# Performance work log

Hardware: AMD Instinct MI355X
Metric: run time of the kernel (lower is better)

## Reference

```python
import jax, jax.numpy as jnp
import numpy as np

N, E, G = 50000, 800000, 128
F_IN, H, NHID, C = 310, 128, 64, 2  # H = 2*nhid
NEG_SLOPE = 0.2


def setup_inputs() -> dict:
    key = jax.random.key(0)
    ks = jax.random.split(key, 16)
    def lin(k, fan_in, shape):
        return (jax.random.normal(k, shape, jnp.float32) / np.sqrt(fan_in)).astype(jnp.float32)
    return {
        "x": jax.random.normal(ks[0], (N, F_IN), jnp.float32),
        "edge_index": jax.random.randint(ks[1], (2, E), 0, N, dtype=jnp.int32),
        "batch": jnp.sort(jax.random.randint(ks[2], (N,), 0, G, dtype=jnp.int32)),
        "W1": lin(ks[3], F_IN, (F_IN, H)),
        "a_src1": lin(ks[4], H, (H,)),
        "a_dst1": lin(ks[5], H, (H,)),
        "b1": jnp.zeros((H,), jnp.float32),
        "W2": lin(ks[6], H, (H, H)),
        "a_src2": lin(ks[7], H, (H,)),
        "a_dst2": lin(ks[8], H, (H,)),
        "b2": jnp.zeros((H,), jnp.float32),
        "fc1_w": lin(ks[9], H, (H, NHID)),
        "fc1_b": jnp.zeros((NHID,), jnp.float32),
        "fc2_w": lin(ks[10], NHID, (NHID, C)),
        "fc2_b": jnp.zeros((C,), jnp.float32),
    }


def _gat(x, src, dst, W, a_src, a_dst, b):
    # PyG GATConv, heads=1: h = xW; e_ij = LeakyReLU(a_src.h_j + a_dst.h_i)
    h = x @ W                               # [N, H]
    asrc = h @ a_src                        # [N]
    adst = h @ a_dst                        # [N]
    e = jax.nn.leaky_relu(asrc[src] + adst[dst], NEG_SLOPE)  # [E']
    # segment softmax over incoming edges of each target node
    m = jax.ops.segment_max(e, dst, num_segments=N)
    ex = jnp.exp(e - m[dst])
    s = jax.ops.segment_sum(ex, dst, num_segments=N)
    w = ex / s[dst]                         # [E']
    out = jax.ops.segment_sum(h[src] * w[:, None], dst, num_segments=N)
    return out + b


def reference(x, edge_index, batch, W1, a_src1, a_dst1, b1,
              W2, a_src2, a_dst2, b2, fc1_w, fc1_b, fc2_w, fc2_b):
    # add self loops (GATConv default add_self_loops=True)
    ar = jnp.arange(N, dtype=edge_index.dtype)
    src = jnp.concatenate([edge_index[0], ar])
    dst = jnp.concatenate([edge_index[1], ar])

    h = jax.nn.selu(_gat(x, src, dst, W1, a_src1, a_dst1, b1))
    h = jax.nn.selu(_gat(h, src, dst, W2, a_src2, a_dst2, b2))

    # global mean pool over graphs
    summed = jax.ops.segment_sum(h, batch, num_segments=G)          # [G, H]
    cnt = jax.ops.segment_sum(jnp.ones((N,), h.dtype), batch, num_segments=G)
    pooled = jax.nn.selu(summed / jnp.maximum(cnt, 1.0)[:, None])

    z = jax.nn.selu(pooled @ fc1_w + fc1_b)  # dropout is identity in eval
    logits = z @ fc2_w + fc2_b
    return jax.nn.log_softmax(logits, axis=-1)
```

## Files before the change

kernel.cpp:

```cpp
#include <hip/hip_runtime.h>
#include <hip/hip_bf16.h>
#include <math.h>

#define NN 50000
#define NE 800000
#define NET (NE + NN)
#define FIN 310
#define HD 128
#define NHID 64
#define NCLS 2
#define NG 128
#define NEG_SLOPE 0.2f
#define KP1 320
#define KP2 128

#define SLOTS 64
#define NPART 8
#define PART_SZ (NN / NPART)
#define EPB 4096
#define NSLICE ((NET + EPB - 1) / EPB)
#define NSC (NSLICE * NPART)
#define GB1 ((NN + 63) / 64)

#define SELU_SCALE 1.0507009873554804934193349852946f
#define SELU_ALPHA 1.6732632423543772848170429916717f

typedef short bf16x8 __attribute__((ext_vector_type(8)));
typedef float f32x4 __attribute__((ext_vector_type(4)));

__device__ __forceinline__ float selu(float x) {
    return SELU_SCALE * (x > 0.f ? x : SELU_ALPHA * (__expf(x) - 1.f));
}
__device__ __forceinline__ float lrelu(float x) {
    return x > 0.f ? x : NEG_SLOPE * x;
}
__device__ __forceinline__ unsigned short f2bf(float f) {
    unsigned int u = __float_as_uint(f);
    u = (u + 0x7fffu + ((u >> 16) & 1u)) >> 16;
    return (unsigned short)u;
}
__device__ __forceinline__ float bf2f(unsigned short b) {
    return __uint_as_float(((unsigned int)b) << 16);
}


__global__ void k_castW(const float* __restrict__ W1, const float* __restrict__ W2,
                        unsigned short* __restrict__ W1p, unsigned short* __restrict__ W2p,
                        int* __restrict__ cursor) {
    int i = blockIdx.x * blockDim.x + threadIdx.x;
    if (i < NN) cursor[i] = 0;
    const int N1 = HD * KP1;
    if (i < N1) {
        int n = i / KP1, k = i % KP1;
        unsigned short v = (k < FIN) ? f2bf(W1[(size_t)k * HD + n]) : (unsigned short)0;
        W1p[((k >> 3) * HD + n) * 8 + (k & 7)] = v;
    } else {
        int j = i - N1;
        if (j < HD * KP2) {
            int n = j / KP2, k = j % KP2;
            W2p[((k >> 3) * HD + n) * 8 + (k & 7)] = f2bf(W2[(size_t)k * HD + n]);
        }
    }
}


#define RGEMM_EPILOGUE                                                         \
    int gr_base = r0 + w * 16 + quad * 4;                                      \
    _Pragma("unroll")                                                          \
    for (int r = 0; r < 4; ++r) {                                              \
        int gr = gr_base + r;                                                  \
        if (gr < M) {                                                          \
            _Pragma("unroll")                                                  \
            for (int nt = 0; nt < 8; ++nt)                                     \
                C[(size_t)gr * HD + nt * 16 + l16] = f2bf(acc[nt][r]);         \
        }                                                                      \
    }                                                                          \
    _Pragma("unroll")                                                          \
    for (int r = 0; r < 4; ++r) {                                              \
        float s1 = 0.f, s2 = 0.f;                                              \
        _Pragma("unroll")                                                      \
        for (int nt = 0; nt < 8; ++nt) {                                       \
            int c = nt * 16 + l16;                                             \
            float v = acc[nt][r];                                              \
            s1 += v * a_src[c];                                                \
            s2 += v * a_dst[c];                                                \
        }                                                                      \
        _Pragma("unroll")                                                      \
        for (int off = 1; off < 16; off <<= 1) {                               \
            s1 += __shfl_xor(s1, off);                                         \
            s2 += __shfl_xor(s2, off);                                         \
        }                                                                      \
        int gr = gr_base + r;                                                  \
        if (l16 == 0 && gr < M) { asrcp[gr] = s1; adstp[gr] = s2; }            \
    }


__global__ __launch_bounds__(256) void k_pre(const float* __restrict__ A,
                                             const unsigned short* __restrict__ Bp,
                                             unsigned short* __restrict__ C,
                                             float* __restrict__ asrcp,
                                             float* __restrict__ adstp,
                                             const float* __restrict__ a_src,
                                             const float* __restrict__ a_dst,
                                             int M,
                                             const int* __restrict__ ei,
                                             int* __restrict__ cursor,
                                             unsigned short* __restrict__ slots) {
    if (blockIdx.x >= GB1) {
        int b = blockIdx.x - GB1;
        int part = b & (NPART - 1);
        int slice = b >> 3;
        int lo = part * PART_SZ;
        int base = slice * EPB + threadIdx.x;
#pragma unroll
        for (int k = 0; k < EPB / 256; ++k) {
            int i = base + k * 256;
            if (i >= NET) break;
            int d = (i < NE) ? ei[NE + i] : (i - NE);
            if ((unsigned)(d - lo) < (unsigned)PART_SZ) {
                int s = (i < NE) ? ei[i] : d;
                int pos = atomicAdd(&cursor[d], 1) & (SLOTS - 1);
                slots[(size_t)d * SLOTS + pos] = (unsigned short)s;
            }
        }
        return;
    }
    int t = threadIdx.x;
    int lane = t & 63, w = t >> 6;
    int quad = lane >> 4, l16 = lane & 15;
    int r0 = blockIdx.x * 64;

    int grow = r0 + w * 16 + l16;
    int arow = min(grow, M - 1);
    const float* aptr = A + (size_t)arow * FIN + quad * 8;

    f32x4 acc[8] = {};
#pragma unroll 2
    for (int k0 = 0; k0 < 288; k0 += 32) {
        const float* ap = aptr + k0;
        float2 f0 = *(const float2*)(ap + 0);
        float2 f1 = *(const float2*)(ap + 2);
        float2 f2 = *(const float2*)(ap + 4);
        float2 f3 = *(const float2*)(ap + 6);
        union { bf16x8 v; unsigned short u[8]; } af;
        af.u[0] = f2bf(f0.x); af.u[1] = f2bf(f0.y);
        af.u[2] = f2bf(f1.x); af.u[3] = f2bf(f1.y);
        af.u[4] = f2bf(f2.x); af.u[5] = f2bf(f2.y);
        af.u[6] = f2bf(f3.x); af.u[7] = f2bf(f3.y);
        const unsigned short* bbase = Bp + ((size_t)(k0 >> 3) + quad) * (HD * 8) + l16 * 8;
#pragma unroll
        for (int nt = 0; nt < 8; ++nt) {
            bf16x8 bfr = *(const bf16x8*)(bbase + nt * 128);
            acc[nt] = __builtin_amdgcn_mfma_f32_16x16x32_bf16(af.v, bfr, acc[nt], 0, 0, 0);
        }
    }
    {
        int kb = 288 + quad * 8;
        union { bf16x8 v; unsigned short u[8]; } af;
#pragma unroll
        for (int j = 0; j < 8; ++j)
            af.u[j] = (kb + j < FIN) ? f2bf(aptr[288 + j]) : (unsigned short)0;
        const unsigned short* bbase = Bp + ((size_t)(288 >> 3) + quad) * (HD * 8) + l16 * 8;
#pragma unroll
        for (int nt = 0; nt < 8; ++nt) {
            bf16x8 bfr = *(const bf16x8*)(bbase + nt * 128);
            acc[nt] = __builtin_amdgcn_mfma_f32_16x16x32_bf16(af.v, bfr, acc[nt], 0, 0, 0);
        }
    }
    RGEMM_EPILOGUE
}


__global__ __launch_bounds__(256) void k_gemm2(const unsigned short* __restrict__ A,
                                               const unsigned short* __restrict__ Bp,
                                               unsigned short* __restrict__ C,
                                               float* __restrict__ asrcp,
                                               float* __restrict__ adstp,
                                               const float* __restrict__ a_src,
                                               const float* __restrict__ a_dst,
                                               int M) {
    int t = threadIdx.x;
    int lane = t & 63, w = t >> 6;
    int quad = lane >> 4, l16 = lane & 15;
    int r0 = blockIdx.x * 64;

    int grow = r0 + w * 16 + l16;
    int arow = min(grow, M - 1);
    const unsigned short* aptr = A + (size_t)arow * KP2 + quad * 8;

    f32x4 acc[8] = {};
#pragma unroll
    for (int k0 = 0; k0 < KP2; k0 += 32) {
        bf16x8 af = *(const bf16x8*)(aptr + k0);
        const unsigned short* bbase = Bp + ((size_t)(k0 >> 3) + quad) * (HD * 8) + l16 * 8;
#pragma unroll
        for (int nt = 0; nt < 8; ++nt) {
            bf16x8 bfr = *(const bf16x8*)(bbase + nt * 128);
            acc[nt] = __builtin_amdgcn_mfma_f32_16x16x32_bf16(af, bfr, acc[nt], 0, 0, 0);
        }
    }
    RGEMM_EPILOGUE
}


__global__ __launch_bounds__(256) void k_gat(const unsigned short* __restrict__ h,
                                             const float* __restrict__ asrc,
                                             const float* __restrict__ adst,
                                             const int* __restrict__ degv,
                                             const unsigned short* __restrict__ slots,
                                             const float* __restrict__ bias,
                                             unsigned short* __restrict__ out) {
    int node = blockIdx.x * 4 + (threadIdx.x >> 6);
    int lane = threadIdx.x & 63;
    if (node >= NN) return;
    int g = lane >> 4, cl = lane & 15;
    int deg = degv[node];
    float adsti = adst[node];

    float2 acc2[4] = {};

    int cnt = min(deg, SLOTS);
    int s_c = 0; float p_c = 0.f;
    if (lane < cnt) {
        s_c = slots[(size_t)node * SLOTS + lane];
        p_c = __expf(lrelu(asrc[s_c] + adsti));
    }
    float den_l = p_c;
    int nt = (cnt + 3) >> 2;
    for (int t = 0; t < nt; t += 2) {
        float pv[2]; uint4 hv[2];
#pragma unroll
        for (int u = 0; u < 2; ++u) {
            int tt = t + u;
            bool valid = tt < nt;
            int e = (4 * tt + g) & 63;
            int s = __shfl(s_c, e);
            float p = __shfl(p_c, e);
            int sa = valid ? s : 0;
            pv[u] = valid ? p : 0.f;
            hv[u] = *(const uint4*)(h + (size_t)sa * HD + cl * 8);
        }
#pragma unroll
        for (int u = 0; u < 2; ++u) {
            float p = pv[u];
            unsigned int w0 = hv[u].x, w1 = hv[u].y, w2 = hv[u].z, w3 = hv[u].w;
            acc2[0].x += p * __uint_as_float(w0 << 16);
            acc2[0].y += p * __uint_as_float(w0 & 0xffff0000u);
            acc2[1].x += p * __uint_as_float(w1 << 16);
            acc2[1].y += p * __uint_as_float(w1 & 0xffff0000u);
            acc2[2].x += p * __uint_as_float(w2 << 16);
            acc2[2].y += p * __uint_as_float(w2 & 0xffff0000u);
            acc2[3].x += p * __uint_as_float(w3 << 16);
            acc2[3].y += p * __uint_as_float(w3 & 0xffff0000u);
        }
    }
#pragma unroll
    for (int k = 0; k < 4; ++k) {
        acc2[k].x += __shfl_xor(acc2[k].x, 16);
        acc2[k].y += __shfl_xor(acc2[k].y, 16);
        acc2[k].x += __shfl_xor(acc2[k].x, 32);
        acc2[k].y += __shfl_xor(acc2[k].y, 32);
    }
#pragma unroll
    for (int off = 32; off; off >>= 1)
        den_l += __shfl_xor(den_l, off);

    if (g == 0) {
        float inv = 1.f / den_l;
        int c0 = cl * 8;
        float4 b0 = *(const float4*)(bias + c0);
        float4 b1 = *(const float4*)(bias + c0 + 4);
        float v0 = selu(acc2[0].x * inv + b0.x);
        float v1 = selu(acc2[0].y * inv + b0.y);
        float v2 = selu(acc2[1].x * inv + b0.z);
        float v3 = selu(acc2[1].y * inv + b0.w);
        float v4 = selu(acc2[2].x * inv + b1.x);
        float v5 = selu(acc2[2].y * inv + b1.y);
        float v6 = selu(acc2[3].x * inv + b1.z);
        float v7 = selu(acc2[3].y * inv + b1.w);
        uint4 pk;
        pk.x = (unsigned int)f2bf(v0) | ((unsigned int)f2bf(v1) << 16);
        pk.y = (unsigned int)f2bf(v2) | ((unsigned int)f2bf(v3) << 16);
        pk.z = (unsigned int)f2bf(v4) | ((unsigned int)f2bf(v5) << 16);
        pk.w = (unsigned int)f2bf(v6) | ((unsigned int)f2bf(v7) << 16);
        *(uint4*)(out + (size_t)node * HD + c0) = pk;
    }
}


__device__ __forceinline__ int lower_bound_i(const int* a, int n, int key) {
    int lo = 0, hi = n;
    while (lo < hi) {
        int mid = (lo + hi) >> 1;
        if (a[mid] < key) lo = mid + 1; else hi = mid;
    }
    return lo;
}

__global__ __launch_bounds__(512) void k_poolfc(const unsigned short* __restrict__ x,
                                                const int* __restrict__ batch,
                                                const float* __restrict__ w1,
                                                const float* __restrict__ b1,
                                                const float* __restrict__ w2,
                                                const float* __restrict__ b2,
                                                float* __restrict__ out) {
    int g = blockIdx.x;
    int t = threadIdx.x;
    __shared__ int lo_s, hi_s;
    __shared__ float red[512];
    __shared__ float pooled_s[128];
    if (t == 0) {
        lo_s = lower_bound_i(batch, NN, g);
        hi_s = lower_bound_i(batch, NN, g + 1);
    }
    __syncthreads();
    int lo = lo_s, hi = hi_s;
    float acc = 0.f;
    for (int n = lo + (t >> 7); n < hi; n += 4)
        acc += bf2f(x[(size_t)n * HD + (t & 127)]);
    red[t] = acc;
    __syncthreads();
    if (t < 128) {
        float v = red[t] + red[t + 128] + red[t + 256] + red[t + 384];
        pooled_s[t] = selu(v / fmaxf((float)(hi - lo), 1.f));
    }
    __syncthreads();
    if (t < 64) {
        float z = 0.f;
#pragma unroll 8
        for (int k = 0; k < HD; ++k) z += pooled_s[k] * w1[k * NHID + t];
        z = selu(z + b1[t]);
        float p0 = z * w2[t * NCLS + 0];
        float p1 = z * w2[t * NCLS + 1];
        for (int off = 32; off; off >>= 1) {
            p0 += __shfl_down(p0, off);
            p1 += __shfl_down(p1, off);
        }
        if (t == 0) {
            float l0 = p0 + b2[0], l1 = p1 + b2[1];
            float m = fmaxf(l0, l1);
            float lse = m + __logf(__expf(l0 - m) + __expf(l1 - m));
            out[g * NCLS + 0] = l0 - lse;
            out[g * NCLS + 1] = l1 - lse;
        }
    }
}


static inline size_t align_up(size_t v, size_t a) { return (v + a - 1) / a * a; }

extern "C" void kernel_launch(void* const* d_in, const int* in_sizes, int n_in,
                              void* d_out, int out_size, void* d_ws, size_t ws_size,
                              hipStream_t stream) {
    const float* x      = (const float*)d_in[0];
    const int*   ei     = (const int*)d_in[1];
    const int*   batch  = (const int*)d_in[2];
    const float* W1     = (const float*)d_in[3];
    const float* a_src1 = (const float*)d_in[4];
    const float* a_dst1 = (const float*)d_in[5];
    const float* b1     = (const float*)d_in[6];
    const float* W2     = (const float*)d_in[7];
    const float* a_src2 = (const float*)d_in[8];
    const float* a_dst2 = (const float*)d_in[9];
    const float* b2     = (const float*)d_in[10];
    const float* fc1_w  = (const float*)d_in[11];
    const float* fc1_b  = (const float*)d_in[12];
    const float* fc2_w  = (const float*)d_in[13];
    const float* fc2_b  = (const float*)d_in[14];
    float* out = (float*)d_out;

    char* ws = (char*)d_ws;
    size_t off = 0;
    unsigned short* h1  = (unsigned short*)(ws + off); off = align_up(off + (size_t)NN * HD * 2, 256);
    unsigned short* o1  = (unsigned short*)(ws + off); off = align_up(off + (size_t)NN * HD * 2, 256);
    float* asrc = (float*)(ws + off); off = align_up(off + (size_t)NN * 4, 256);
    float* adst = (float*)(ws + off); off = align_up(off + (size_t)NN * 4, 256);
    int* cursor = (int*)(ws + off);   off = align_up(off + (size_t)NN * 4, 256);
    unsigned short* slots = (unsigned short*)(ws + off); off = align_up(off + (size_t)NN * SLOTS * 2, 256);
    unsigned short* W1p = (unsigned short*)(ws + off); off = align_up(off + (size_t)HD * KP1 * 2, 256);
    unsigned short* W2p = (unsigned short*)(ws + off); off = align_up(off + (size_t)HD * KP2 * 2, 256);
    (void)ws_size;

    k_castW<<<(HD * (KP1 + KP2) + 255) / 256, 256, 0, stream>>>(W1, W2, W1p, W2p, cursor);

    k_pre<<<GB1 + NSC, 256, 0, stream>>>(x, W1p, h1, asrc, adst, a_src1, a_dst1, NN,
                                         ei, cursor, slots);

    k_gat<<<(NN + 3) / 4, 256, 0, stream>>>(h1, asrc, adst, cursor, slots, b1, o1);

    k_gemm2<<<GB1, 256, 0, stream>>>(o1, W2p, h1, asrc, adst, a_src2, a_dst2, NN);
    k_gat<<<(NN + 3) / 4, 256, 0, stream>>>(h1, asrc, adst, cursor, slots, b2, o1);

    k_poolfc<<<NG, 512, 0, stream>>>(o1, batch, fc1_w, fc1_b, fc2_w, fc2_b, out);
}
```

Before: 288.0 us.

## Split x bf16 cast into separate kernel, rebalance edge scatter, deepen GAT gather

Adds a k_mix kernel that converts x to a padded bf16 buffer while running part of the edge-slot scatter. The first-layer GEMM then reads bf16 rows through a shared templated routine instead of converting fp32 inline. The remaining scatter slices stay co-scheduled with that GEMM. The GAT aggregation loop now keeps four gathered rows in flight instead of two, raising memory-level parallelism. In exchange it adds an extra kernel launch, extra write and read traffic for the bf16 copy of x, and more registers in the gather loop.

Measured after the change: 298.1 us. 3.5% more time.

```diff
diff --git a/kernel.cpp b/kernel.cpp
--- a/kernel.cpp
+++ b/kernel.cpp
@@ -19,8 +19,11 @@
 #define PART_SZ (NN / NPART)
 #define EPB 4096
 #define NSLICE ((NET + EPB - 1) / EPB)
-#define NSC (NSLICE * NPART)
+#define SSPLIT 104
+#define NSC_MIX (SSPLIT * 8)
+#define NSC_PRE ((NSLICE - SSPLIT) * 8)
 #define GB1 ((NN + 63) / 64)
+#define CXB ((NN * 40 + 255) / 256)
 
 #define SELU_SCALE 1.0507009873554804934193349852946f
 #define SELU_ALPHA 1.6732632423543772848170429916717f
@@ -59,6 +62,26 @@
         if (j < HD * KP2) {
             int n = j / KP2, k = j % KP2;
             W2p[((k >> 3) * HD + n) * 8 + (k & 7)] = f2bf(W2[(size_t)k * HD + n]);
+        }
+    }
+}
+
+
+__device__ __forceinline__ void scatter_body(int slice, const int* __restrict__ ei,
+                                             int* __restrict__ cursor,
+                                             unsigned short* __restrict__ slots,
+                                             int part) {
+    int lo = part * PART_SZ;
+    int base = slice * EPB + threadIdx.x;
+#pragma unroll
+    for (int k = 0; k < EPB / 256; ++k) {
+        int i = base + k * 256;
+        if (i >= NET) break;
+        int d = (i < NE) ? ei[NE + i] : (i - NE);
+        if ((unsigned)(d - lo) < (unsigned)PART_SZ) {
+            int s = (i < NE) ? ei[i] : d;
+            int pos = atomicAdd(&cursor[d], 1) & (SLOTS - 1);
+            slots[(size_t)d * SLOTS + pos] = (unsigned short)s;
         }
     }
 }
@@ -95,7 +118,74 @@
     }
 
 
-__global__ __launch_bounds__(256) void k_pre(const float* __restrict__ A,
+template <int KP>
+__device__ __forceinline__ void gemm_rows(const unsigned short* __restrict__ A,
+                                          const unsigned short* __restrict__ Bp,
+                                          unsigned short* __restrict__ C,
+                                          float* __restrict__ asrcp,
+                                          float* __restrict__ adstp,
+                                          const float* __restrict__ a_src,
+                                          const float* __restrict__ a_dst,
+                                          int M) {
+    int t = threadIdx.x;
+    int lane = t & 63, w = t >> 6;
+    int quad = lane >> 4, l16 = lane & 15;
+    int r0 = blockIdx.x * 64;
+
+    int grow = r0 + w * 16 + l16;
+    int arow = min(grow, M - 1);
+    const unsigned short* aptr = A + (size_t)arow * KP + quad * 8;
+
+    f32x4 acc[8] = {};
+#pragma unroll
+    for (int k0 = 0; k0 < KP; k0 += 32) {
+        bf16x8 af = *(const bf16x8*)(aptr + k0);
+        const unsigned short* bbase = Bp + ((size_t)(k0 >> 3) + quad) * (HD * 8) + l16 * 8;
+#pragma unroll
+        for (int nt = 0; nt < 8; ++nt) {
+            bf16x8 bfr = *(const bf16x8*)(bbase + nt * 128);
+            acc[nt] = __builtin_amdgcn_mfma_f32_16x16x32_bf16(af, bfr, acc[nt], 0, 0, 0);
+        }
+    }
+    RGEMM_EPILOGUE
+}
+
+
+__global__ __launch_bounds__(256) void k_mix(const float* __restrict__ x,
+                                             unsigned short* __restrict__ xb,
+                                             const int* __restrict__ ei,
+                                             int* __restrict__ cursor,
+                                             unsigned short* __restrict__ slots) {
+    if (blockIdx.x < NSC_MIX) {
+        int part = (blockIdx.x + 2) & 7;
+        scatter_body(blockIdx.x >> 3, ei, cursor, slots, part);
+        return;
+    }
+    int j = (blockIdx.x - NSC_MIX) * 256 + threadIdx.x;
+    int row = j / 40;
+    if (row >= NN) return;
+    int c0 = (j - row * 40) * 8;
+    const float* xp = x + (size_t)row * FIN + c0;
+    union { bf16x8 v; unsigned short u[8]; } o;
+    if (c0 + 8 <= FIN) {
+        float2 f0 = *(const float2*)(xp + 0);
+        float2 f1 = *(const float2*)(xp + 2);
+        float2 f2 = *(const float2*)(xp + 4);
+        float2 f3 = *(const float2*)(xp + 6);
+        o.u[0] = f2bf(f0.x); o.u[1] = f2bf(f0.y);
+        o.u[2] = f2bf(f1.x); o.u[3] = f2bf(f1.y);
+        o.u[4] = f2bf(f2.x); o.u[5] = f2bf(f2.y);
+        o.u[6] = f2bf(f3.x); o.u[7] = f2bf(f3.y);
+    } else {
+#pragma unroll
+        for (int q = 0; q < 8; ++q)
+            o.u[q] = (c0 + q < FIN) ? f2bf(xp[q]) : (unsigned short)0;
+    }
+    *(bf16x8*)(xb + (size_t)row * KP1 + c0) = o.v;
+}
+
+
+__global__ __launch_bounds__(256) void k_pre(const unsigned short* __restrict__ xb,
                                              const unsigned short* __restrict__ Bp,
                                              unsigned short* __restrict__ C,
                                              float* __restrict__ asrcp,
@@ -108,66 +198,11 @@
                                              unsigned short* __restrict__ slots) {
     if (blockIdx.x >= GB1) {
         int b = blockIdx.x - GB1;
-        int part = b & (NPART - 1);
-        int slice = b >> 3;
-        int lo = part * PART_SZ;
-        int base = slice * EPB + threadIdx.x;
-#pragma unroll
-        for (int k = 0; k < EPB / 256; ++k) {
-            int i = base + k * 256;
-            if (i >= NET) break;
-            int d = (i < NE) ? ei[NE + i] : (i - NE);
-            if ((unsigned)(d - lo) < (unsigned)PART_SZ) {
-                int s = (i < NE) ? ei[i] : d;
-                int pos = atomicAdd(&cursor[d], 1) & (SLOTS - 1);
-                slots[(size_t)d * SLOTS + pos] = (unsigned short)s;
-            }
-        }
+        int part = (blockIdx.x + 2) & 7;
+        scatter_body(SSPLIT + (b >> 3), ei, cursor, slots, part);
         return;
     }
-    int t = threadIdx.x;
-    int lane = t & 63, w = t >> 6;
-    int quad = lane >> 4, l16 = lane & 15;
-    int r0 = blockIdx.x * 64;
-
-    int grow = r0 + w * 16 + l16;
-    int arow = min(grow, M - 1);
-    const float* aptr = A + (size_t)arow * FIN + quad * 8;
-
-    f32x4 acc[8] = {};
-#pragma unroll 2
-    for (int k0 = 0; k0 < 288; k0 += 32) {
-        const float* ap = aptr + k0;
-        float2 f0 = *(const float2*)(ap + 0);
-        float2 f1 = *(const float2*)(ap + 2);
-        float2 f2 = *(const float2*)(ap + 4);
-        float2 f3 = *(const float2*)(ap + 6);
-        union { bf16x8 v; unsigned short u[8]; } af;
-        af.u[0] = f2bf(f0.x); af.u[1] = f2bf(f0.y);
-        af.u[2] = f2bf(f1.x); af.u[3] = f2bf(f1.y);
-        af.u[4] = f2bf(f2.x); af.u[5] = f2bf(f2.y);
-        af.u[6] = f2bf(f3.x); af.u[7] = f2bf(f3.y);
-        const unsigned short* bbase = Bp + ((size_t)(k0 >> 3) + quad) * (HD * 8) + l16 * 8;
-#pragma unroll
-        for (int nt = 0; nt < 8; ++nt) {
-            bf16x8 bfr = *(const bf16x8*)(bbase + nt * 128);
-            acc[nt] = __builtin_amdgcn_mfma_f32_16x16x32_bf16(af.v, bfr, acc[nt], 0, 0, 0);
-        }
-    }
-    {
-        int kb = 288 + quad * 8;
-        union { bf16x8 v; unsigned short u[8]; } af;
-#pragma unroll
-        for (int j = 0; j < 8; ++j)
-            af.u[j] = (kb + j < FIN) ? f2bf(aptr[288 + j]) : (unsigned short)0;
-        const unsigned short* bbase = Bp + ((size_t)(288 >> 3) + quad) * (HD * 8) + l16 * 8;
-#pragma unroll
-        for (int nt = 0; nt < 8; ++nt) {
-            bf16x8 bfr = *(const bf16x8*)(bbase + nt * 128);
-            acc[nt] = __builtin_amdgcn_mfma_f32_16x16x32_bf16(af.v, bfr, acc[nt], 0, 0, 0);
-        }
-    }
-    RGEMM_EPILOGUE
+    gemm_rows<KP1>(xb, Bp, C, asrcp, adstp, a_src, a_dst, M);
 }
 
 
@@ -179,27 +214,7 @@
                                                const float* __restrict__ a_src,
                                                const float* __restrict__ a_dst,
                                                int M) {
-    int t = threadIdx.x;
-    int lane = t & 63, w = t >> 6;
-    int quad = lane >> 4, l16 = lane & 15;
-    int r0 = blockIdx.x * 64;
-
-    int grow = r0 + w * 16 + l16;
-    int arow = min(grow, M - 1);
-    const unsigned short* aptr = A + (size_t)arow * KP2 + quad * 8;
-
-    f32x4 acc[8] = {};
-#pragma unroll
-    for (int k0 = 0; k0 < KP2; k0 += 32) {
-        bf16x8 af = *(const bf16x8*)(aptr + k0);
-        const unsigned short* bbase = Bp + ((size_t)(k0 >> 3) + quad) * (HD * 8) + l16 * 8;
-#pragma unroll
-        for (int nt = 0; nt < 8; ++nt) {
-            bf16x8 bfr = *(const bf16x8*)(bbase + nt * 128);
-            acc[nt] = __builtin_amdgcn_mfma_f32_16x16x32_bf16(af, bfr, acc[nt], 0, 0, 0);
-        }
-    }
-    RGEMM_EPILOGUE
+    gemm_rows<KP2>(A, Bp, C, asrcp, adstp, a_src, a_dst, M);
 }
 
 
@@ -227,10 +242,10 @@
     }
     float den_l = p_c;
     int nt = (cnt + 3) >> 2;
-    for (int t = 0; t < nt; t += 2) {
-        float pv[2]; uint4 hv[2];
-#pragma unroll
-        for (int u = 0; u < 2; ++u) {
+    for (int t = 0; t < nt; t += 4) {
+        float pv[4]; uint4 hv[4];
+#pragma unroll
+        for (int u = 0; u < 4; ++u) {
             int tt = t + u;
             bool valid = tt < nt;
             int e = (4 * tt + g) & 63;
@@ -241,7 +256,7 @@
             hv[u] = *(const uint4*)(h + (size_t)sa * HD + cl * 8);
         }
 #pragma unroll
-        for (int u = 0; u < 2; ++u) {
+        for (int u = 0; u < 4; ++u) {
             float p = pv[u];
             unsigned int w0 = hv[u].x, w1 = hv[u].y, w2 = hv[u].z, w3 = hv[u].w;
             acc2[0].x += p * __uint_as_float(w0 << 16);
@@ -379,12 +394,15 @@
     unsigned short* slots = (unsigned short*)(ws + off); off = align_up(off + (size_t)NN * SLOTS * 2, 256);
     unsigned short* W1p = (unsigned short*)(ws + off); off = align_up(off + (size_t)HD * KP1 * 2, 256);
     unsigned short* W2p = (unsigned short*)(ws + off); off = align_up(off + (size_t)HD * KP2 * 2, 256);
+    unsigned short* xb  = (unsigned short*)(ws + off); off = align_up(off + (size_t)NN * KP1 * 2, 256);
     (void)ws_size;
 
     k_castW<<<(HD * (KP1 + KP2) + 255) / 256, 256, 0, stream>>>(W1, W2, W1p, W2p, cursor);
 
-    k_pre<<<GB1 + NSC, 256, 0, stream>>>(x, W1p, h1, asrc, adst, a_src1, a_dst1, NN,
-                                         ei, cursor, slots);
+    k_mix<<<NSC_MIX + CXB, 256, 0, stream>>>(x, xb, ei, cursor, slots);
+
+    k_pre<<<GB1 + NSC_PRE, 256, 0, stream>>>(xb, W1p, h1, asrc, adst, a_src1, a_dst1, NN,
+                                             ei, cursor, slots);
 
     k_gat<<<(NN + 3) / 4, 256, 0, stream>>>(h1, asrc, adst, cursor, slots, b1, o1);
 
```
